# Kernel optimization log

Measured on AMD Instinct MI355X. Metric: run time of the kernel, lower is better.

Reference implementation:

```python
import jax, jax.numpy as jnp
import numpy as np

B, H, E, K = 8192, 1024, 8, 2


def setup_inputs() -> dict:
    key = jax.random.key(0)
    k1, k2, k3 = jax.random.split(key, 3)
    x = jax.random.normal(k1, (B, H), dtype=jnp.float32)
    gate_w = jax.random.normal(k2, (H, E), dtype=jnp.float32) / np.sqrt(H)
    expert_w = jax.random.normal(k3, (E, H, H), dtype=jnp.float32) / np.sqrt(H)
    return {"x": x, "gate_w": gate_w, "expert_w": expert_w}


def reference(x, gate_w, expert_w):
    # Gate: logits over experts, top-k routing, softmax over the k selected logits
    logits = x @ gate_w                               # [B, E]
    top_w, top_idx = jax.lax.top_k(logits, K)         # [B, K]
    top_w = jax.nn.softmax(top_w, axis=-1)            # softmax over the K selected
    # Combine weights scattered back to [B, E]; zero for unselected experts
    combine = jnp.zeros((x.shape[0], expert_w.shape[0]), dtype=x.dtype)
    combine = combine.at[jnp.arange(x.shape[0])[:, None], top_idx].add(top_w)
    # Expert GEMMs (dense dispatch reference: every expert on every token,
    # masked/weighted by combine; mathematically identical to gather/scatter)
    expert_out = jnp.einsum('bh,eho->beo', x, expert_w)   # [B, E, H]
    out = jnp.einsum('be,beo->bo', combine, expert_out)   # [B, H]
    return out
```

## Files before the change

### kernel.cpp

```cpp
#include <hip/hip_runtime.h>
#include <hip/hip_bf16.h>
#include <stdint.h>

#define B_TOK 8192
#define H_DIM 1024
#define E_NUM 8
#define NSLOT (2 * B_TOK)

typedef __attribute__((ext_vector_type(8))) short short8;
typedef __attribute__((ext_vector_type(4))) float floatx4;

__device__ __forceinline__ unsigned short f32_to_bf16_rne(float f) {
  union { float f; uint32_t u; } v; v.f = f;
  uint32_t u = v.u;
  uint32_t r = u + 0x7FFFu + ((u >> 16) & 1u);
  return (unsigned short)(r >> 16);
}
__device__ __forceinline__ float bf16_to_f32(unsigned short s) {
  union { uint32_t u; float f; } v; v.u = ((uint32_t)s) << 16;
  return v.f;
}

__global__ __launch_bounds__(256) void prep_kernel(const float* __restrict__ x,
                                                   const float* __restrict__ gw,
                                                   const float* __restrict__ ew,
                                                   unsigned short* __restrict__ xb,
                                                   unsigned short* __restrict__ wt,
                                                   int2* __restrict__ re,
                                                   float2* __restrict__ rw) {
  __shared__ float smem[E_NUM * 1028];
  int bid = blockIdx.x;
  int tid = threadIdx.x;
  if (bid < 2048) {
    float (*tile)[65] = (float(*)[65])smem;
    int e = bid >> 8;
    int n0 = ((bid >> 4) & 15) * 64, k0 = (bid & 15) * 64;
    const float* wb = ew + ((size_t)e * H_DIM + k0) * H_DIM + n0;
    unsigned short* wtb = wt + ((size_t)e * H_DIM + n0) * H_DIM + k0;
    int rr = tid >> 4, c4 = tid & 15;
#pragma unroll
    for (int j = 0; j < 4; ++j) {
      int r = rr + j * 16;
      float4 v = *(const float4*)(wb + (size_t)r * H_DIM + c4 * 4);
      tile[c4 * 4 + 0][r] = v.x;
      tile[c4 * 4 + 1][r] = v.y;
      tile[c4 * 4 + 2][r] = v.z;
      tile[c4 * 4 + 3][r] = v.w;
    }
    __syncthreads();
#pragma unroll
    for (int j = 0; j < 4; ++j) {
      int nr = rr + j * 16;
      float4 v = *(const float4*)&tile[nr][c4 * 4];
      ushort4 o;
      o.x = f32_to_bf16_rne(v.x); o.y = f32_to_bf16_rne(v.y);
      o.z = f32_to_bf16_rne(v.z); o.w = f32_to_bf16_rne(v.w);
      *(ushort4*)(wtb + (size_t)nr * H_DIM + c4 * 4) = o;
    }
  } else {
    int rb = bid - 2048;
    float (*gws)[1028] = (float(*)[1028])smem;
#pragma unroll
    for (int it = 0; it < 8; ++it) {
      int i4 = it * 256 + tid;
      float4 v = ((const float4*)gw)[i4];
      int h = i4 >> 1, e0 = (i4 & 1) * 4;
      gws[e0 + 0][h] = v.x;
      gws[e0 + 1][h] = v.y;
      gws[e0 + 2][h] = v.z;
      gws[e0 + 3][h] = v.w;
    }
    __syncthreads();
    int wid = tid >> 6, lane = tid & 63;
    for (int t = 0; t < 4; ++t) {
      int b = rb * 16 + wid * 4 + t;
      const float4* xr = (const float4*)(x + (size_t)b * H_DIM);
      ushort4* xbr = (ushort4*)(xb + (size_t)b * H_DIM);
      float acc[E_NUM];
#pragma unroll
      for (int e = 0; e < E_NUM; e++) acc[e] = 0.f;
#pragma unroll
      for (int it = 0; it < 4; ++it) {
        int c4 = it * 64 + lane;
        float4 v = xr[c4];
        ushort4 o;
        o.x = f32_to_bf16_rne(v.x); o.y = f32_to_bf16_rne(v.y);
        o.z = f32_to_bf16_rne(v.z); o.w = f32_to_bf16_rne(v.w);
        xbr[c4] = o;
        int h = c4 * 4;
#pragma unroll
        for (int e = 0; e < E_NUM; e++) {
          float4 g = *(const float4*)&gws[e][h];
          acc[e] += v.x * g.x + v.y * g.y + v.z * g.z + v.w * g.w;
        }
      }
#pragma unroll
      for (int e = 0; e < E_NUM; e++) {
#pragma unroll
        for (int off = 32; off; off >>= 1) acc[e] += __shfl_xor(acc[e], off, 64);
      }
      if (lane == 0) {
        int e0 = 0; float v0 = acc[0];
#pragma unroll
        for (int e = 1; e < E_NUM; e++) if (acc[e] > v0) { v0 = acc[e]; e0 = e; }
        int e1 = -1; float v1 = -1e30f;
#pragma unroll
        for (int e = 0; e < E_NUM; e++) if (e != e0 && acc[e] > v1) { v1 = acc[e]; e1 = e; }
        float s = expf(v1 - v0);
        float w0 = 1.0f / (1.0f + s);
        re[b] = make_int2(e0, e1);
        rw[b] = make_float2(w0, s * w0);
      }
    }
  }
}

__global__ __launch_bounds__(1024) void compact_kernel(const int2* __restrict__ re,
                                                       int* __restrict__ slot_tok,
                                                       int* __restrict__ yslot,
                                                       int* __restrict__ ebase,
                                                       int* __restrict__ ecnt) {
  __shared__ int wcnt[8][16];
  __shared__ int bless[16];
  int e = blockIdx.x;
  int tid = threadIdx.x, wid = tid >> 6, lane = tid & 63;
  int cless = 0;
  int flag[8];
  unsigned long long mm[8];
#pragma unroll
  for (int it = 0; it < 8; ++it) {
    int2 ee = re[it * 1024 + tid];
    cless += (ee.x < e) + (ee.y < e);
    bool f0 = (ee.x == e), f1 = (ee.y == e);
    flag[it] = f0 ? 1 : (f1 ? 2 : 0);
    mm[it] = __ballot(f0 || f1);
    if (lane == 0) wcnt[it][wid] = __popcll(mm[it]);
  }
#pragma unroll
  for (int off = 32; off; off >>= 1) cless += __shfl_xor(cless, off, 64);
  if (lane == 0) bless[wid] = cless;
  __syncthreads();
  int base = 0;
#pragma unroll
  for (int i = 0; i < 16; ++i) base += bless[i];
  int run = 0;
#pragma unroll
  for (int it = 0; it < 8; ++it) {
    int wbase = 0, total = 0;
#pragma unroll
    for (int i = 0; i < 16; ++i) { int v = wcnt[it][i]; if (i < wid) wbase += v; total += v; }
    if (flag[it]) {
      int pre = __popcll(mm[it] & ((1ull << lane) - 1ull));
      int s = base + run + wbase + pre;
      int t = it * 1024 + tid;
      slot_tok[s] = t;
      yslot[2 * t + (flag[it] == 1 ? 0 : 1)] = s;
    }
    run += total;
  }
  if (tid == 0) { ebase[e] = base; ecnt[e] = run; }
}

__device__ __forceinline__ void async_ld16(const void* g, void* l) {
  __builtin_amdgcn_global_load_lds((const __attribute__((address_space(1))) void*)g,
                                   (__attribute__((address_space(3))) void*)l, 16, 0, 0);
}

__global__ __launch_bounds__(256, 3) void moe_gemm_kernel(
    const unsigned short* __restrict__ xb,
    const unsigned short* __restrict__ wt,
    const int* __restrict__ ebase,
    const int* __restrict__ ecnt,
    const int* __restrict__ slot_tok,
    unsigned short* __restrict__ y) {
  int e = blockIdx.z;
  int c = ecnt[e];
  int m_idx = ((blockIdx.y >> 3) << 3) + blockIdx.x;
  int n_idx = blockIdx.y & 7;
  int m0 = m_idx * 128;
  if (m0 >= c) return;
  int base = ebase[e];
  int n0 = n_idx * 128;

  __shared__ __align__(16) unsigned short As[128 * 64];
  __shared__ __align__(16) unsigned short Bs[128 * 64];

  int tid = threadIdx.x, wid = tid >> 6, lane = tid & 63;
  int rloc = lane >> 3;
  int cl = lane & 7;
  const int* st = slot_tok + base;

  const unsigned short* gA[4];
  const unsigned short* gB[4];
  unsigned short* lA[4];
  unsigned short* lB[4];
#pragma unroll
  for (int j = 0; j < 4; ++j) {
    int rl = wid * 32 + j * 8 + rloc;
    int g = (cl ^ (rl & 7)) * 8;
    int ra = min(m0 + rl, c - 1);
    gA[j] = xb + (size_t)st[ra] * H_DIM + g;
    gB[j] = wt + ((size_t)e * H_DIM + n0 + rl) * H_DIM + g;
    lA[j] = As + (wid * 32 + j * 8) * 64;
    lB[j] = Bs + (wid * 32 + j * 8) * 64;
  }

  floatx4 acc[4][4];
#pragma unroll
  for (int a = 0; a < 4; ++a)
#pragma unroll
    for (int b = 0; b < 4; ++b)
#pragma unroll
      for (int q = 0; q < 4; ++q) acc[a][b][q] = 0.0f;

  int wm = (wid >> 1) * 64, wn = (wid & 1) * 64;
  int mr = lane & 15, kg = lane >> 4;
  int sw = mr & 7;

  for (int ks = 0; ks < 16; ++ks) {
    __syncthreads();
#pragma unroll
    for (int j = 0; j < 4; ++j) {
      async_ld16(gA[j], lA[j]);
      async_ld16(gB[j], lB[j]);
    }
#pragma unroll
    for (int j = 0; j < 4; ++j) { gA[j] += 64; gB[j] += 64; }
    __syncthreads();
#pragma unroll
    for (int kk = 0; kk < 2; ++kk) {
      int cb = ((kk * 4 + kg) ^ sw) * 8;
      short8 af[4], bfr[4];
#pragma unroll
      for (int t = 0; t < 4; ++t) {
        af[t]  = *(const short8*)(const void*)(As + (wm + t * 16 + mr) * 64 + cb);
        bfr[t] = *(const short8*)(const void*)(Bs + (wn + t * 16 + mr) * 64 + cb);
      }
#pragma unroll
      for (int tm = 0; tm < 4; ++tm)
#pragma unroll
        for (int tn = 0; tn < 4; ++tn)
          acc[tm][tn] = __builtin_amdgcn_mfma_f32_16x16x32_bf16(af[tm], bfr[tn], acc[tm][tn], 0, 0, 0);
    }
  }

#pragma unroll
  for (int tm = 0; tm < 4; ++tm) {
#pragma unroll
    for (int q = 0; q < 4; ++q) {
      int r = m0 + wm + tm * 16 + kg * 4 + q;
      if (r < c) {
        unsigned short* yrow = y + (size_t)(base + r) * H_DIM + n0 + wn + mr;
#pragma unroll
        for (int tn = 0; tn < 4; ++tn) yrow[tn * 16] = f32_to_bf16_rne(acc[tm][tn][q]);
      }
    }
  }
}

__global__ __launch_bounds__(256) void combine_kernel(const unsigned short* __restrict__ y,
                                                      const int* __restrict__ yslot,
                                                      const float2* __restrict__ rw,
                                                      float* __restrict__ out) {
  int wid = threadIdx.x >> 6, lane = threadIdx.x & 63;
  int t = blockIdx.x * 4 + wid;
  int s0 = yslot[2 * t], s1 = yslot[2 * t + 1];
  float2 w = rw[t];
  const ushort4* y0 = (const ushort4*)(y + (size_t)s0 * H_DIM);
  const ushort4* y1 = (const ushort4*)(y + (size_t)s1 * H_DIM);
  float4* o = (float4*)(out + (size_t)t * H_DIM);
  ushort4 a[4], b[4];
#pragma unroll
  for (int j = 0; j < 4; ++j) {
    int i = j * 64 + lane;
    a[j] = y0[i];
    b[j] = y1[i];
  }
#pragma unroll
  for (int j = 0; j < 4; ++j) {
    int i = j * 64 + lane;
    float4 r;
    r.x = w.x * bf16_to_f32(a[j].x) + w.y * bf16_to_f32(b[j].x);
    r.y = w.x * bf16_to_f32(a[j].y) + w.y * bf16_to_f32(b[j].y);
    r.z = w.x * bf16_to_f32(a[j].z) + w.y * bf16_to_f32(b[j].z);
    r.w = w.x * bf16_to_f32(a[j].w) + w.y * bf16_to_f32(b[j].w);
    o[i] = r;
  }
}

extern "C" void kernel_launch(void* const* d_in, const int* in_sizes, int n_in,
                              void* d_out, int out_size, void* d_ws, size_t ws_size,
                              hipStream_t stream) {
  const float* x  = (const float*)d_in[0];
  const float* gw = (const float*)d_in[1];
  const float* ew = (const float*)d_in[2];
  float* out = (float*)d_out;

  char* ws = (char*)d_ws;
  unsigned short* xb = (unsigned short*)ws;
  unsigned short* wt = (unsigned short*)(ws + (size_t)16 * 1024 * 1024);
  unsigned short* y  = (unsigned short*)(ws + (size_t)32 * 1024 * 1024);
  char* p = ws + (size_t)64 * 1024 * 1024;
  int2*   re       = (int2*)p;
  float2* rw       = (float2*)(p + (64 << 10));
  int*    slot_tok = (int*)(p + (128 << 10));
  int*    yslot    = (int*)(p + (192 << 10));
  int*    ebase    = (int*)(p + (256 << 10));
  int*    ecnt     = (int*)(p + (256 << 10) + 64);

  prep_kernel<<<2560, 256, 0, stream>>>(x, gw, ew, xb, wt, re, rw);
  compact_kernel<<<E_NUM, 1024, 0, stream>>>(re, slot_tok, yslot, ebase, ecnt);
  moe_gemm_kernel<<<dim3(8, 24, E_NUM), 256, 0, stream>>>(
      xb, wt, ebase, ecnt, slot_tok, y);
  combine_kernel<<<B_TOK / 4, 256, 0, stream>>>(y, yslot, rw, out);
}
```

Baseline: 169.6 us.

## Fuse expert compaction into prep kernel via per-expert atomic slot allocation

Removes the separate compact_kernel launch. Each gating block now ranks its 16 tokens per expert in shared memory and claims slot ranges from a per-expert global atomic counter. Each expert's region sits at a fixed offset of e*MAXC, so ebase is no longer needed. This saves a kernel launch and a serial 8-block pass, but adds a memset, makes slot order nondeterministic, and assumes no expert receives more than 2560 tokens.

```diff
diff --git a/kernel.cpp b/kernel.cpp
--- a/kernel.cpp
+++ b/kernel.cpp
@@ -5,7 +5,7 @@
 #define B_TOK 8192
 #define H_DIM 1024
 #define E_NUM 8
-#define NSLOT (2 * B_TOK)
+#define MAXC 2560
 
 typedef __attribute__((ext_vector_type(8))) short short8;
 typedef __attribute__((ext_vector_type(4))) float floatx4;
@@ -26,9 +26,14 @@
                                                    const float* __restrict__ ew,
                                                    unsigned short* __restrict__ xb,
                                                    unsigned short* __restrict__ wt,
-                                                   int2* __restrict__ re,
-                                                   float2* __restrict__ rw) {
+                                                   float2* __restrict__ rw,
+                                                   int* __restrict__ slot_tok,
+                                                   int* __restrict__ yslot,
+                                                   int* __restrict__ ecnt) {
   __shared__ float smem[E_NUM * 1028];
+  __shared__ int sse[32];
+  __shared__ int srank[32];
+  __shared__ int sbase[E_NUM];
   int bid = blockIdx.x;
   int tid = threadIdx.x;
   if (bid < 2048) {
@@ -73,7 +78,8 @@
     __syncthreads();
     int wid = tid >> 6, lane = tid & 63;
     for (int t = 0; t < 4; ++t) {
-      int b = rb * 16 + wid * 4 + t;
+      int i = wid * 4 + t;
+      int b = rb * 16 + i;
       const float4* xr = (const float4*)(x + (size_t)b * H_DIM);
       ushort4* xbr = (ushort4*)(xb + (size_t)b * H_DIM);
       float acc[E_NUM];
@@ -108,57 +114,40 @@
         for (int e = 0; e < E_NUM; e++) if (e != e0 && acc[e] > v1) { v1 = acc[e]; e1 = e; }
         float s = expf(v1 - v0);
         float w0 = 1.0f / (1.0f + s);
-        re[b] = make_int2(e0, e1);
         rw[b] = make_float2(w0, s * w0);
-      }
-    }
-  }
-}
-
-__global__ __launch_bounds__(1024) void compact_kernel(const int2* __restrict__ re,
-                                                       int* __restrict__ slot_tok,
-                                                       int* __restrict__ yslot,
-                                                       int* __restrict__ ebase,
-                                                       int* __restrict__ ecnt) {
-  __shared__ int wcnt[8][16];
-  __shared__ int bless[16];
-  int e = blockIdx.x;
-  int tid = threadIdx.x, wid = tid >> 6, lane = tid & 63;
-  int cless = 0;
-  int flag[8];
-  unsigned long long mm[8];
-#pragma unroll
-  for (int it = 0; it < 8; ++it) {
-    int2 ee = re[it * 1024 + tid];
-    cless += (ee.x < e) + (ee.y < e);
-    bool f0 = (ee.x == e), f1 = (ee.y == e);
-    flag[it] = f0 ? 1 : (f1 ? 2 : 0);
-    mm[it] = __ballot(f0 || f1);
-    if (lane == 0) wcnt[it][wid] = __popcll(mm[it]);
-  }
-#pragma unroll
-  for (int off = 32; off; off >>= 1) cless += __shfl_xor(cless, off, 64);
-  if (lane == 0) bless[wid] = cless;
-  __syncthreads();
-  int base = 0;
-#pragma unroll
-  for (int i = 0; i < 16; ++i) base += bless[i];
-  int run = 0;
-#pragma unroll
-  for (int it = 0; it < 8; ++it) {
-    int wbase = 0, total = 0;
-#pragma unroll
-    for (int i = 0; i < 16; ++i) { int v = wcnt[it][i]; if (i < wid) wbase += v; total += v; }
-    if (flag[it]) {
-      int pre = __popcll(mm[it] & ((1ull << lane) - 1ull));
-      int s = base + run + wbase + pre;
-      int t = it * 1024 + tid;
-      slot_tok[s] = t;
-      yslot[2 * t + (flag[it] == 1 ? 0 : 1)] = s;
-    }
-    run += total;
-  }
-  if (tid == 0) { ebase[e] = base; ecnt[e] = run; }
+        sse[2 * i] = e0;
+        sse[2 * i + 1] = e1;
+      }
+    }
+    __syncthreads();
+    if (tid < 16) {
+      int e0 = sse[2 * tid], e1 = sse[2 * tid + 1];
+      int r0 = 0, r1 = 0;
+      for (int j = 0; j < tid; ++j) {
+        int a = sse[2 * j], bb = sse[2 * j + 1];
+        r0 += (a == e0) + (bb == e0);
+        r1 += (a == e1) + (bb == e1);
+      }
+      srank[2 * tid] = r0;
+      srank[2 * tid + 1] = r1;
+    }
+    if (tid < E_NUM) {
+      int cnt = 0;
+      for (int j = 0; j < 16; ++j) cnt += (sse[2 * j] == tid) + (sse[2 * j + 1] == tid);
+      sbase[tid] = cnt ? atomicAdd(&ecnt[tid], cnt) : 0;
+    }
+    __syncthreads();
+    if (tid < 16) {
+      int tok = rb * 16 + tid;
+      int e0 = sse[2 * tid], e1 = sse[2 * tid + 1];
+      int s0 = e0 * MAXC + sbase[e0] + srank[2 * tid];
+      int s1 = e1 * MAXC + sbase[e1] + srank[2 * tid + 1];
+      slot_tok[s0] = tok;
+      slot_tok[s1] = tok;
+      yslot[2 * tok] = s0;
+      yslot[2 * tok + 1] = s1;
+    }
+  }
 }
 
 __device__ __forceinline__ void async_ld16(const void* g, void* l) {
@@ -169,7 +158,6 @@
 __global__ __launch_bounds__(256, 3) void moe_gemm_kernel(
     const unsigned short* __restrict__ xb,
     const unsigned short* __restrict__ wt,
-    const int* __restrict__ ebase,
     const int* __restrict__ ecnt,
     const int* __restrict__ slot_tok,
     unsigned short* __restrict__ y) {
@@ -179,7 +167,7 @@
   int n_idx = blockIdx.y & 7;
   int m0 = m_idx * 128;
   if (m0 >= c) return;
-  int base = ebase[e];
+  int base = e * MAXC;
   int n0 = n_idx * 128;
 
   __shared__ __align__(16) unsigned short As[128 * 64];
@@ -300,17 +288,14 @@
   unsigned short* xb = (unsigned short*)ws;
   unsigned short* wt = (unsigned short*)(ws + (size_t)16 * 1024 * 1024);
   unsigned short* y  = (unsigned short*)(ws + (size_t)32 * 1024 * 1024);
-  char* p = ws + (size_t)64 * 1024 * 1024;
-  int2*   re       = (int2*)p;
-  float2* rw       = (float2*)(p + (64 << 10));
-  int*    slot_tok = (int*)(p + (128 << 10));
+  char* p = ws + (size_t)72 * 1024 * 1024;
+  float2* rw       = (float2*)p;
+  int*    slot_tok = (int*)(p + (64 << 10));
   int*    yslot    = (int*)(p + (192 << 10));
-  int*    ebase    = (int*)(p + (256 << 10));
-  int*    ecnt     = (int*)(p + (256 << 10) + 64);
-
-  prep_kernel<<<2560, 256, 0, stream>>>(x, gw, ew, xb, wt, re, rw);
-  compact_kernel<<<E_NUM, 1024, 0, stream>>>(re, slot_tok, yslot, ebase, ecnt);
-  moe_gemm_kernel<<<dim3(8, 24, E_NUM), 256, 0, stream>>>(
-      xb, wt, ebase, ecnt, slot_tok, y);
+  int*    ecnt     = (int*)(p + (256 << 10));
+
+  hipMemsetAsync(ecnt, 0, E_NUM * sizeof(int), stream);
+  prep_kernel<<<2560, 256, 0, stream>>>(x, gw, ew, xb, wt, rw, slot_tok, yslot, ecnt);
+  moe_gemm_kernel<<<dim3(8, 24, E_NUM), 256, 0, stream>>>(xb, wt, ecnt, slot_tok, y);
   combine_kernel<<<B_TOK / 4, 256, 0, stream>>>(y, yslot, rw, out);
 }
```

Measured after the change: 166.6 us. About the same (-1.8%).
